# Performance work log

Hardware: AMD Instinct MI355X
Metric: run time of the kernel (lower is better)

## Reference

```python
import jax, jax.numpy as jnp
import numpy as np
import math

DIM = 1024
N_HEADS = 16
HEAD_DIM = DIM // N_HEADS  # 64
GROUP = 128
B, T = 2, 2048
ROPE_THETA = 10000.0


def bitlinear(x, w, group_size=GROUP):
    """BitLinear (BitNet b1.58 style) forward: per-group ternary weight quant +
    per-token int8 absmax activation quant. STE is irrelevant in fwd-only."""
    O, I = w.shape
    wg = w.reshape(O, I // group_size, group_size)
    ws = jnp.mean(jnp.abs(wg), axis=-1, keepdims=True) + 1e-5
    wq = (jnp.clip(jnp.round(wg / ws), -1.0, 1.0) * ws).reshape(O, I)
    s = 127.0 / (jnp.max(jnp.abs(x), axis=-1, keepdims=True) + 1e-5)
    xq = jnp.clip(jnp.round(x * s), -128.0, 127.0) / s
    return jnp.einsum('bti,oi->bto', xq, wq)


def rope(x, cos, sin):
    # x: [B,T,H,D]; cos/sin: [T,D/2]; complex mult on interleaved pairs
    xs = x.reshape(*x.shape[:-1], -1, 2)
    xe, xo = xs[..., 0], xs[..., 1]
    c = cos[None, :, None, :]
    s = sin[None, :, None, :]
    oe = xe * c - xo * s
    oo = xe * s + xo * c
    return jnp.stack([oe, oo], axis=-1).reshape(x.shape)


def setup_inputs() -> dict:
    key = jax.random.key(0)
    ks = jax.random.split(key, 5)
    x = jax.random.normal(ks[0], (B, T, DIM), dtype=jnp.float32)
    wq_w = jax.random.normal(ks[1], (DIM, DIM), dtype=jnp.float32) * 0.02
    wk_w = jax.random.normal(ks[2], (DIM, DIM), dtype=jnp.float32) * 0.02
    wv_w = jax.random.normal(ks[3], (DIM, DIM), dtype=jnp.float32) * 0.02
    wo_w = jax.random.normal(ks[4], (DIM, DIM), dtype=jnp.float32) * 0.02
    # precompute freqs_cis (as cos/sin) like standard RoPE
    inv = 1.0 / (ROPE_THETA ** (np.arange(0, HEAD_DIM, 2, dtype=np.float32) / HEAD_DIM))
    ang = np.arange(T, dtype=np.float32)[:, None] * inv[None, :]  # [T, D/2]
    return {
        'x': x,
        'cos': jnp.asarray(np.cos(ang)),
        'sin': jnp.asarray(np.sin(ang)),
        'wq_w': wq_w, 'wk_w': wk_w, 'wv_w': wv_w, 'wo_w': wo_w,
    }


def reference(x, cos, sin, wq_w, wk_w, wv_w, wo_w):
    Bb, Tt, _ = x.shape
    q = bitlinear(x, wq_w).reshape(Bb, Tt, N_HEADS, HEAD_DIM)
    k = bitlinear(x, wk_w).reshape(Bb, Tt, N_HEADS, HEAD_DIM)
    v = bitlinear(x, wv_w).reshape(Bb, Tt, N_HEADS, HEAD_DIM)
    q = rope(q, cos, sin)
    k = rope(k, cos, sin)
    # [B,H,T,D]
    q = q.transpose(0, 2, 1, 3)
    k = k.transpose(0, 2, 1, 3)
    v = v.transpose(0, 2, 1, 3)
    attn = jnp.einsum('bhqd,bhkd->bhqk', q, k) / math.sqrt(HEAD_DIM)
    causal = jnp.tril(jnp.ones((Tt, Tt), dtype=bool))
    attn = jnp.where(causal[None, None], attn, -jnp.inf)
    attn = jax.nn.softmax(attn, axis=-1)
    out = jnp.einsum('bhqk,bhkd->bhqd', attn, v)
    out = out.transpose(0, 2, 1, 3).reshape(Bb, Tt, -1)
    return bitlinear(out, wo_w)
```

## Files before the change

kernel.cpp:

```cpp
#include <hip/hip_runtime.h>
#include <math.h>

#define DIM   1024
#define NH    16
#define HD    64
#define GRP   128
#define BB    2
#define TT    2048
#define MROWS (BB*TT)

typedef __attribute__((ext_vector_type(8))) short s16x8;
typedef __attribute__((ext_vector_type(4))) float f32x4;
typedef __attribute__((ext_vector_type(4))) int   i32x4;
typedef __attribute__((ext_vector_type(16))) int  i32x16;

__device__ inline float wave_max(float v){
    for(int off=32; off; off>>=1) v = fmaxf(v, __shfl_xor(v, off));
    return v;
}

__device__ inline unsigned short f2bf(float x){
    union { float f; unsigned u; } v; v.f = x;
    unsigned r = v.u + 0x7fffu + ((v.u >> 16) & 1u);
    return (unsigned short)(r >> 16);
}

#if __has_builtin(__builtin_amdgcn_cvt_pk_bf16_f32)
typedef __bf16 bf16x2 __attribute__((ext_vector_type(2)));
__device__ inline unsigned pk2(float a, float b){
    union { bf16x2 v; unsigned u; } c;
    c.v = __builtin_amdgcn_cvt_pk_bf16_f32(a, b);
    return c.u;
}
#else
__device__ inline unsigned pk2(float a, float b){
    return (unsigned)f2bf(a) | ((unsigned)f2bf(b) << 16);
}
#endif

#if __has_builtin(__builtin_amdgcn_exp2f)
__device__ inline float fexp2(float x){ return __builtin_amdgcn_exp2f(x); }
#else
__device__ inline float fexp2(float x){ return exp2f(x); }
#endif

__device__ inline i32x16 zero16(){
    i32x16 z;
    #pragma unroll
    for(int i=0;i<16;i++) z[i]=0;
    return z;
}

__device__ inline void gload16(const void* g, void* l){
    __builtin_amdgcn_global_load_lds((const __attribute__((address_space(1))) unsigned int*)g,
                                     (__attribute__((address_space(3))) unsigned int*)l, 16, 0, 0);
}

__global__ __launch_bounds__(256) void quant_w4(const float* __restrict__ w0,
                                                const float* __restrict__ w1,
                                                const float* __restrict__ w2,
                                                const float* __restrict__ w3,
                                                char* __restrict__ w8,
                                                float* __restrict__ wsall){
    int blk = blockIdx.x;
    int widx = blk >> 8;
    const float* w = (widx==0)?w0 : (widx==1)?w1 : (widx==2)?w2 : w3;
    int tid = threadIdx.x;
    int gloc = (blk & 255)*32 + (tid >> 3);
    int j = tid & 7;
    const float* p = w + (size_t)gloc*GRP;
    float r = 0.f;
    #pragma unroll
    for(int i=0;i<16;i++) r += fabsf(p[8*i + j]);
    r += __shfl_xor(r, 1);
    r += __shfl_xor(r, 2);
    r += __shfl_xor(r, 4);
    float ws = r/(float)GRP + 1e-5f;
    if (j == 0) wsall[widx*8192 + gloc] = ws;
    int* q = (int*)(w8 + (size_t)widx*1048576 + (size_t)gloc*GRP);
    int i0 = j*16;
    #pragma unroll
    for(int c4=0;c4<4;c4++){
        float4 v = *(const float4*)(p + i0 + c4*4);
        int b0 = (int)fminf(fmaxf(rintf(v.x/ws),-1.f),1.f);
        int b1 = (int)fminf(fmaxf(rintf(v.y/ws),-1.f),1.f);
        int b2 = (int)fminf(fmaxf(rintf(v.z/ws),-1.f),1.f);
        int b3 = (int)fminf(fmaxf(rintf(v.w/ws),-1.f),1.f);
        q[j*4 + c4] = (b0&0xff) | ((b1&0xff)<<8) | ((b2&0xff)<<16) | ((b3&0xff)<<24);
    }
}

__global__ __launch_bounds__(256) void quant_x_i8(const float* __restrict__ x,
                                                  char* __restrict__ xq8,
                                                  float* __restrict__ srow){
    int row = blockIdx.x;
    int tid = threadIdx.x;
    const float* p = x + (size_t)row*DIM;
    float4 v = *(const float4*)(p + tid*4);
    float m = fmaxf(fmaxf(fabsf(v.x),fabsf(v.y)), fmaxf(fabsf(v.z),fabsf(v.w)));
    m = wave_max(m);
    __shared__ float red[4];
    if ((tid&63)==0) red[tid>>6] = m;
    __syncthreads();
    m = fmaxf(fmaxf(red[0],red[1]), fmaxf(red[2],red[3]));
    float s = 127.f/(m+1e-5f);
    int a0 = (int)fminf(fmaxf(rintf(v.x*s),-128.f),127.f);
    int a1 = (int)fminf(fmaxf(rintf(v.y*s),-128.f),127.f);
    int a2 = (int)fminf(fmaxf(rintf(v.z*s),-128.f),127.f);
    int a3 = (int)fminf(fmaxf(rintf(v.w*s),-128.f),127.f);
    int pk = (a0&0xff) | ((a1&0xff)<<8) | ((a2&0xff)<<16) | ((a3&0xff)<<24);
    ((int*)xq8)[(size_t)row*256 + tid] = pk;
    if (tid==0) srow[row] = s;
}

__global__ __launch_bounds__(256) void gemm_i8(const char* __restrict__ A8,
                                               const char* __restrict__ W8,
                                               const float* __restrict__ wsb,
                                               const float* __restrict__ srow,
                                               float* __restrict__ C){
    __shared__ __align__(16) char As[2][8192];
    __shared__ __align__(16) char Bs[2][16384];
    int tid = threadIdx.x;
    int w = tid >> 6, lane = tid & 63;
    int wm = w & 1, wn = w >> 1;
    int m0 = blockIdx.y*64, n0 = blockIdx.x*128;
    int l31 = lane & 31, lh = lane >> 5;

    float wsr[2][8];
    #pragma unroll
    for(int jt=0; jt<2; jt++){
        int col = n0 + (wn*2+jt)*32 + l31;
        float4 q0 = *(const float4*)(wsb + (size_t)col*8);
        float4 q1 = *(const float4*)(wsb + (size_t)col*8 + 4);
        wsr[jt][0]=q0.x; wsr[jt][1]=q0.y; wsr[jt][2]=q0.z; wsr[jt][3]=q0.w;
        wsr[jt][4]=q1.x; wsr[jt][5]=q1.y; wsr[jt][6]=q1.z; wsr[jt][7]=q1.w;
    }

    float facc[2][16];
    #pragma unroll
    for(int b=0;b<2;b++)
        #pragma unroll
        for(int r=0;r<16;r++) facc[b][r]=0.f;

    int row8 = lane >> 3;
    int scw  = (lane&7) ^ ((lane>>3)&7);
    const char* Ab = A8 + (size_t)m0*1024;
    const char* Bb = W8 + (size_t)n0*1024;

    {
        #pragma unroll
        for(int r=0;r<2;r++){
            int j = w*2 + r;
            gload16(Ab + (size_t)(j*8 + row8)*1024 + scw*16, As[0] + j*1024);
        }
        #pragma unroll
        for(int r=0;r<4;r++){
            int j = w*4 + r;
            gload16(Bb + (size_t)(j*8 + row8)*1024 + scw*16, Bs[0] + j*1024);
        }
    }

    #pragma unroll
    for(int g=0; g<8; g++){
        __syncthreads();
        if (g+1 < 8){
            int nb = (g+1)&1;
            #pragma unroll
            for(int r=0;r<2;r++){
                int j = w*2 + r;
                gload16(Ab + (size_t)(j*8 + row8)*1024 + (g+1)*128 + scw*16, As[nb] + j*1024);
            }
            #pragma unroll
            for(int r=0;r<4;r++){
                int j = w*4 + r;
                gload16(Bb + (size_t)(j*8 + row8)*1024 + (g+1)*128 + scw*16, Bs[nb] + j*1024);
            }
        }
        const char* Ac = As[g&1];
        const char* Bc = Bs[g&1];

        i32x16 iacc[2];
        iacc[0]=zero16(); iacc[1]=zero16();
        #pragma unroll
        for(int s=0; s<4; s++){
            int cw = s*2 + lh;
            int rlA = wm*32 + l31;
            i32x4 afr = *(const i32x4*)(Ac + (rlA*8 + (cw ^ (rlA&7)))*16);
            #pragma unroll
            for(int jt=0; jt<2; jt++){
                int rlB = (wn*2+jt)*32 + l31;
                i32x4 bfr = *(const i32x4*)(Bc + (rlB*8 + (cw ^ (rlB&7)))*16);
                iacc[jt] = __builtin_amdgcn_mfma_i32_32x32x32_i8(afr, bfr, iacc[jt], 0, 0, 0);
            }
        }
        #pragma unroll
        for(int jt=0; jt<2; jt++)
            #pragma unroll
            for(int r=0;r<16;r++)
                facc[jt][r] += (float)iacc[jt][r] * wsr[jt][g];
    }

    #pragma unroll
    for(int r=0; r<16; r++){
        int rowl = wm*32 + (r&3) + 8*(r>>2) + 4*lh;
        float sv = srow[m0 + rowl];
        #pragma unroll
        for(int jt=0; jt<2; jt++){
            int col = n0 + (wn*2+jt)*32 + l31;
            C[(size_t)(m0+rowl)*DIM + col] = facc[jt][r] / sv;
        }
    }
}

#define QSC 0.18033688011112042f
__global__ __launch_bounds__(256) void pack_qk(const float* __restrict__ qb,
                                               const float* __restrict__ kb,
                                               const float* __restrict__ cosb,
                                               const float* __restrict__ sinb,
                                               unsigned short* __restrict__ Qh,
                                               char* __restrict__ Kf){
    int idx = blockIdx.x*blockDim.x + threadIdx.x;
    int bt = idx >> 9;
    int r  = idx & 511;
    int h  = r >> 5;
    int p  = r & 31;
    int b  = bt >> 11;
    int t  = bt & (TT-1);
    int bh = b*NH + h;
    float c = cosb[t*32+p], s = sinb[t*32+p];
    size_t src = (size_t)bt*DIM + h*HD + 2*p;
    float q0 = qb[src], q1 = qb[src+1];
    float k0 = kb[src], k1 = kb[src+1];
    float qe = (q0*c - q1*s)*QSC, qo = (q0*s + q1*c)*QSC;
    float ke = k0*c - k1*s,       ko = k0*s + k1*c;
    size_t qdst = ((size_t)bh*TT + t)*HD + 2*p;
    *(ushort2*)(Qh + qdst) = make_ushort2(f2bf(qe), f2bf(qo));
    int kt = t >> 6, tl = t & 63;
    int f = tl >> 4, mm = tl & 15;
    int cc = p >> 4, gg = (p >> 2) & 3, j2 = (p & 3)*2;
    size_t kdst = ((size_t)(bh*32 + kt)*512 + f*128 + cc*64 + gg*16 + mm)*16 + j2*2;
    *(ushort2*)(Kf + kdst) = make_ushort2(f2bf(ke), f2bf(ko));
}

__global__ __launch_bounds__(256) void pack_v(const float* __restrict__ vb,
                                              char* __restrict__ Vf){
    __shared__ float st[64][65];
    int blk = blockIdx.x;
    int kt = blk & 31;
    int bh = blk >> 5;
    int b  = bh >> 4;
    int h  = bh & 15;
    int tid = threadIdx.x;
    #pragma unroll
    for(int rep=0; rep<16; rep++){
        int idx = rep*256 + tid;
        int tl = idx >> 6, dv = idx & 63;
        st[tl][dv] = vb[(size_t)(b*TT + kt*64 + tl)*DIM + h*HD + dv];
    }
    __syncthreads();
    char* base = Vf + ((size_t)blk*512)*16;
    #pragma unroll
    for(int rep=0; rep<2; rep++){
        int e = rep*256 + tid;
        int f = e >> 7, cc = (e >> 6) & 1, gg = (e >> 4) & 3, mm = e & 15;
        int dv = 16*f + mm;
        int tb = 8*gg + 32*cc;
        unsigned short sh[8];
        #pragma unroll
        for(int j=0;j<8;j++) sh[j] = f2bf(st[tb+j][dv]);
        *(s16x8*)(base + (size_t)e*16) = *(s16x8*)sh;
    }
}

__global__ __launch_bounds__(256) void attn_mfma3(const unsigned short* __restrict__ Qh,
                                                  const char* __restrict__ Kf,
                                                  const char* __restrict__ Vf,
                                                  float* __restrict__ ao){
    __shared__ s16x8 Kbuf[2][512];
    __shared__ s16x8 Vbuf[2][512];
    int blk = blockIdx.x;
    int qt = 31 - (blk >> 5);
    int bh = blk & 31;
    int b  = bh >> 4;
    int tid = threadIdx.x;
    int w = tid >> 6, lane = tid & 63;
    int m = lane & 15, g = lane >> 4;
    int q = qt*64 + w*16 + m;

    const unsigned short* Qhead = Qh + (size_t)bh*TT*HD;
    const char* Kbase = Kf + (size_t)bh*32*8192;
    const char* Vbase = Vf + (size_t)bh*32*8192;

    s16x8 Qf0 = *(const s16x8*)(Qhead + (size_t)q*HD + g*8);
    s16x8 Qf1 = *(const s16x8*)(Qhead + (size_t)q*HD + g*8 + 32);

    f32x4 Of[4] = {f32x4{0,0,0,0}, f32x4{0,0,0,0}, f32x4{0,0,0,0}, f32x4{0,0,0,0}};
    float mrow = -1e30f, lrow = 0.f;

    #pragma unroll
    for(int r=0;r<2;r++){
        gload16(Kbase + ((r*4 + w)*64 + lane)*16, (char*)Kbuf[0] + (r*4 + w)*1024);
        gload16(Vbase + ((r*4 + w)*64 + lane)*16, (char*)Vbuf[0] + (r*4 + w)*1024);
    }

    for(int kt=0; kt<=qt; kt++){
        __syncthreads();
        if (kt < qt){
            int nb = (kt+1)&1;
            size_t goff = (size_t)(kt+1)*8192;
            #pragma unroll
            for(int r=0;r<2;r++){
                gload16(Kbase + goff + ((r*4 + w)*64 + lane)*16, (char*)Kbuf[nb] + (r*4 + w)*1024);
                gload16(Vbase + goff + ((r*4 + w)*64 + lane)*16, (char*)Vbuf[nb] + (r*4 + w)*1024);
            }
        }
        const s16x8* Kc = Kbuf[kt&1];
        const s16x8* Vc = Vbuf[kt&1];

        f32x4 S[4];
        #pragma unroll
        for(int f=0; f<4; f++){
            s16x8 k0 = Kc[(f*2+0)*64 + lane];
            s16x8 k1 = Kc[(f*2+1)*64 + lane];
            f32x4 acc = {0,0,0,0};
            acc = __builtin_amdgcn_mfma_f32_16x16x32_bf16(k0, Qf0, acc, 0, 0, 0);
            acc = __builtin_amdgcn_mfma_f32_16x16x32_bf16(k1, Qf1, acc, 0, 0, 0);
            S[f] = acc;
        }

        float p[4][4];
        float mloc = -1e30f;
        if (kt == qt){
            #pragma unroll
            for(int f=0; f<4; f++)
                #pragma unroll
                for(int r=0; r<4; r++){
                    int key = 16*f + 4*g + r;
                    float s = (qt*64 + key > q) ? -1e30f : S[f][r];
                    p[f][r] = s;
                    mloc = fmaxf(mloc, s);
                }
        } else {
            #pragma unroll
            for(int f=0; f<4; f++)
                #pragma unroll
                for(int r=0; r<4; r++){
                    p[f][r] = S[f][r];
                    mloc = fmaxf(mloc, S[f][r]);
                }
        }
        mloc = fmaxf(mloc, __shfl_xor(mloc, 16));
        mloc = fmaxf(mloc, __shfl_xor(mloc, 32));
        float mn = fmaxf(mrow, mloc);
        float alpha = fexp2(mrow - mn);
        float ps = 0.f;
        #pragma unroll
        for(int f=0; f<4; f++)
            #pragma unroll
            for(int r=0; r<4; r++){
                float e = fexp2(p[f][r] - mn);
                p[f][r] = e;
                ps += e;
            }
        ps += __shfl_xor(ps, 16);
        ps += __shfl_xor(ps, 32);
        lrow = lrow*alpha + ps;
        mrow = mn;

        #pragma unroll
        for(int f2=0; f2<4; f2++)
            #pragma unroll
            for(int r=0; r<4; r++) Of[f2][r] *= alpha;

        unsigned pp0[4], pp1[4];
        #pragma unroll
        for(int f=0; f<4; f++){
            pp0[f] = pk2(p[f][0], p[f][1]);
            pp1[f] = pk2(p[f][2], p[f][3]);
        }

        int src0 = m + 16*(2*(g&1));
        int src1 = src0 + 16;
        bool hi = (g >= 2);
        #pragma unroll
        for(int c=0; c<2; c++){
            unsigned a0 = (unsigned)__shfl((int)pp0[2*c],   src0);
            unsigned a1 = (unsigned)__shfl((int)pp0[2*c+1], src0);
            unsigned b0 = hi ? a1 : a0;
            unsigned a2 = (unsigned)__shfl((int)pp1[2*c],   src0);
            unsigned a3 = (unsigned)__shfl((int)pp1[2*c+1], src0);
            unsigned b1 = hi ? a3 : a2;
            unsigned a4 = (unsigned)__shfl((int)pp0[2*c],   src1);
            unsigned a5 = (unsigned)__shfl((int)pp0[2*c+1], src1);
            unsigned b2 = hi ? a5 : a4;
            unsigned a6 = (unsigned)__shfl((int)pp1[2*c],   src1);
            unsigned a7 = (unsigned)__shfl((int)pp1[2*c+1], src1);
            unsigned b3 = hi ? a7 : a6;
            union { unsigned u[4]; s16x8 v; } Bf;
            Bf.u[0]=b0; Bf.u[1]=b1; Bf.u[2]=b2; Bf.u[3]=b3;
            #pragma unroll
            for(int f2=0; f2<4; f2++){
                s16x8 vf = Vc[(f2*2+c)*64 + lane];
                Of[f2] = __builtin_amdgcn_mfma_f32_16x16x32_bf16(vf, Bf.v, Of[f2], 0, 0, 0);
            }
        }
    }

    float invl = 1.0f / lrow;
    size_t obase = (size_t)(b*TT + q)*DIM + (bh & 15)*HD;
    #pragma unroll
    for(int f2=0; f2<4; f2++)
        #pragma unroll
        for(int r=0; r<4; r++)
            ao[obase + 16*f2 + 4*g + r] = Of[f2][r]*invl;
}

extern "C" void kernel_launch(void* const* d_in, const int* in_sizes, int n_in,
                              void* d_out, int out_size, void* d_ws, size_t ws_size,
                              hipStream_t stream){
    const float* x    = (const float*)d_in[0];
    const float* cosb = (const float*)d_in[1];
    const float* sinb = (const float*)d_in[2];
    const float* wq_w = (const float*)d_in[3];
    const float* wk_w = (const float*)d_in[4];
    const float* wv_w = (const float*)d_in[5];
    const float* wo_w = (const float*)d_in[6];
    float* out = (float*)d_out;

    char*  cw = (char*)d_ws;
    const size_t MB = 1048576;
    char*  w8all = cw;
    float* wsall = (float*)(cw + 4*MB);
    float* srow1 = wsall + 4*8192;
    float* srow2 = srow1 + 4096;
    char*  xq8   = cw + 5*MB;
    char*  xq8_2 = cw + 9*MB;
    float* qb    = (float*)(cw + 13*MB);
    float* kb    = (float*)(cw + 29*MB);
    float* vb    = (float*)(cw + 45*MB);
    unsigned short* Qh = (unsigned short*)(cw + 61*MB);
    char*  Kf    = cw + 69*MB;
    char*  Vf    = cw + 13*MB;
    float* ao    = kb;

    quant_w4<<<1024, 256, 0, stream>>>(wq_w, wk_w, wv_w, wo_w, w8all, wsall);
    quant_x_i8<<<MROWS, 256, 0, stream>>>(x, xq8, srow1);

    dim3 gg(DIM/128, MROWS/64);
    gemm_i8<<<gg, 256, 0, stream>>>(xq8, w8all + 0*MB, wsall + 0*8192, srow1, qb);
    gemm_i8<<<gg, 256, 0, stream>>>(xq8, w8all + 1*MB, wsall + 1*8192, srow1, kb);
    gemm_i8<<<gg, 256, 0, stream>>>(xq8, w8all + 2*MB, wsall + 2*8192, srow1, vb);

    pack_qk<<<(MROWS*512)/256, 256, 0, stream>>>(qb, kb, cosb, sinb, Qh, Kf);
    pack_v<<<BB*NH*(TT/64), 256, 0, stream>>>(vb, Vf);

    attn_mfma3<<<1024, 256, 0, stream>>>(Qh, Kf, Vf, ao);

    quant_x_i8<<<MROWS, 256, 0, stream>>>(ao, xq8_2, srow2);
    gemm_i8<<<gg, 256, 0, stream>>>(xq8_2, w8all + 3*MB, wsall + 3*8192, srow2, out);
}
```

Measured before the change: 248.0 us.

## Fuse quant kernels, QKV GEMMs with RoPE/pack, and split-K causal attention

Merges weight and activation quantization into one launch. Fuses the three QKV GEMMs into a single grid whose epilogue applies RoPE and writes bf16 Q/K/V directly in the attention layouts, removing the fp32 intermediates and the pack kernels. Splits long causal query tiles into two key-range halves with a separate merge kernel to balance work across blocks. In exchange it adds scattered 2-byte stores in the GEMM epilogue and partial-result traffic for the merge.

```diff
diff --git a/kernel.cpp b/kernel.cpp
--- a/kernel.cpp
+++ b/kernel.cpp
@@ -56,37 +56,62 @@
                                      (__attribute__((address_space(3))) unsigned int*)l, 16, 0, 0);
 }
 
-__global__ __launch_bounds__(256) void quant_w4(const float* __restrict__ w0,
-                                                const float* __restrict__ w1,
-                                                const float* __restrict__ w2,
-                                                const float* __restrict__ w3,
-                                                char* __restrict__ w8,
-                                                float* __restrict__ wsall){
+#define QSC 0.18033688011112042f
+
+__global__ __launch_bounds__(256) void quant_all(const float* __restrict__ x,
+                                                 const float* __restrict__ w0,
+                                                 const float* __restrict__ w1,
+                                                 const float* __restrict__ w2,
+                                                 const float* __restrict__ w3,
+                                                 char* __restrict__ w8,
+                                                 float* __restrict__ wsall,
+                                                 char* __restrict__ xq8,
+                                                 float* __restrict__ srow){
     int blk = blockIdx.x;
-    int widx = blk >> 8;
-    const float* w = (widx==0)?w0 : (widx==1)?w1 : (widx==2)?w2 : w3;
     int tid = threadIdx.x;
-    int gloc = (blk & 255)*32 + (tid >> 3);
-    int j = tid & 7;
-    const float* p = w + (size_t)gloc*GRP;
-    float r = 0.f;
-    #pragma unroll
-    for(int i=0;i<16;i++) r += fabsf(p[8*i + j]);
-    r += __shfl_xor(r, 1);
-    r += __shfl_xor(r, 2);
-    r += __shfl_xor(r, 4);
-    float ws = r/(float)GRP + 1e-5f;
-    if (j == 0) wsall[widx*8192 + gloc] = ws;
-    int* q = (int*)(w8 + (size_t)widx*1048576 + (size_t)gloc*GRP);
-    int i0 = j*16;
-    #pragma unroll
-    for(int c4=0;c4<4;c4++){
-        float4 v = *(const float4*)(p + i0 + c4*4);
-        int b0 = (int)fminf(fmaxf(rintf(v.x/ws),-1.f),1.f);
-        int b1 = (int)fminf(fmaxf(rintf(v.y/ws),-1.f),1.f);
-        int b2 = (int)fminf(fmaxf(rintf(v.z/ws),-1.f),1.f);
-        int b3 = (int)fminf(fmaxf(rintf(v.w/ws),-1.f),1.f);
-        q[j*4 + c4] = (b0&0xff) | ((b1&0xff)<<8) | ((b2&0xff)<<16) | ((b3&0xff)<<24);
+    if (blk < 1024){
+        int widx = blk >> 8;
+        const float* w = (widx==0)?w0 : (widx==1)?w1 : (widx==2)?w2 : w3;
+        int gloc = (blk & 255)*32 + (tid >> 3);
+        int j = tid & 7;
+        const float* p = w + (size_t)gloc*GRP;
+        float r = 0.f;
+        #pragma unroll
+        for(int i=0;i<16;i++) r += fabsf(p[8*i + j]);
+        r += __shfl_xor(r, 1);
+        r += __shfl_xor(r, 2);
+        r += __shfl_xor(r, 4);
+        float ws = r/(float)GRP + 1e-5f;
+        if (j == 0) wsall[widx*8192 + gloc] = ws;
+        int* q = (int*)(w8 + (size_t)widx*1048576 + (size_t)gloc*GRP);
+        int i0 = j*16;
+        #pragma unroll
+        for(int c4=0;c4<4;c4++){
+            float4 v = *(const float4*)(p + i0 + c4*4);
+            int b0 = (int)fminf(fmaxf(rintf(v.x/ws),-1.f),1.f);
+            int b1 = (int)fminf(fmaxf(rintf(v.y/ws),-1.f),1.f);
+            int b2 = (int)fminf(fmaxf(rintf(v.z/ws),-1.f),1.f);
+            int b3 = (int)fminf(fmaxf(rintf(v.w/ws),-1.f),1.f);
+            q[j*4 + c4] = (b0&0xff) | ((b1&0xff)<<8) | ((b2&0xff)<<16) | ((b3&0xff)<<24);
+        }
+    } else {
+        int row = blk - 1024;
+        const float* p = x + (size_t)row*DIM;
+        float4 v = *(const float4*)(p + tid*4);
+        float m = fmaxf(fmaxf(fabsf(v.x),fabsf(v.y)), fmaxf(fabsf(v.z),fabsf(v.w)));
+        m = wave_max(m);
+        __shared__ float red[4];
+        if ((tid&63)==0) red[tid>>6] = m;
+        __syncthreads();
+        m = fmaxf(fmaxf(red[0],red[1]), fmaxf(red[2],red[3]));
+        float s = 127.f/(m+1e-5f);
+        int a0 = (int)fminf(fmaxf(rintf(v.x*s),-128.f),127.f);
+        int a1 = (int)fminf(fmaxf(rintf(v.y*s),-128.f),127.f);
+        int a2 = (int)fminf(fmaxf(rintf(v.z*s),-128.f),127.f);
+        int a3 = (int)fminf(fmaxf(rintf(v.w*s),-128.f),127.f);
+        int pk = (a0&0xff) | ((a1&0xff)<<8) | ((a2&0xff)<<16) | ((a3&0xff)<<24);
+        ((int*)xq8)[(size_t)row*256 + tid] = pk;
+        if (tid==0) srow[row] = s;
     }
 }
 
@@ -113,6 +138,161 @@
     if (tid==0) srow[row] = s;
 }
 
+__global__ __launch_bounds__(256) void gemm_qkv(const char* __restrict__ A8,
+                                                const char* __restrict__ w8all,
+                                                const float* __restrict__ wsall,
+                                                const float* __restrict__ srow,
+                                                const float* __restrict__ cosb,
+                                                const float* __restrict__ sinb,
+                                                unsigned short* __restrict__ Qh,
+                                                unsigned short* __restrict__ Kf,
+                                                unsigned short* __restrict__ Vf){
+    __shared__ __align__(16) char As[2][8192];
+    __shared__ __align__(16) char Bs[2][16384];
+    int nt = blockIdx.x;
+    int widx = nt >> 3;
+    int n0 = (nt & 7)*128;
+    int m0 = blockIdx.y*64;
+    const char* W8 = w8all + (size_t)widx*1048576;
+    const float* wsb = wsall + widx*8192;
+
+    int tid = threadIdx.x;
+    int w = tid >> 6, lane = tid & 63;
+    int wm = w & 1, wn = w >> 1;
+    int l31 = lane & 31, lh = lane >> 5;
+
+    float wsr[2][8];
+    #pragma unroll
+    for(int jt=0; jt<2; jt++){
+        int col = n0 + (wn*2+jt)*32 + l31;
+        float4 q0 = *(const float4*)(wsb + (size_t)col*8);
+        float4 q1 = *(const float4*)(wsb + (size_t)col*8 + 4);
+        wsr[jt][0]=q0.x; wsr[jt][1]=q0.y; wsr[jt][2]=q0.z; wsr[jt][3]=q0.w;
+        wsr[jt][4]=q1.x; wsr[jt][5]=q1.y; wsr[jt][6]=q1.z; wsr[jt][7]=q1.w;
+    }
+
+    float facc[2][16];
+    #pragma unroll
+    for(int b=0;b<2;b++)
+        #pragma unroll
+        for(int r=0;r<16;r++) facc[b][r]=0.f;
+
+    int row8 = lane >> 3;
+    int scw  = (lane&7) ^ ((lane>>3)&7);
+    const char* Ab = A8 + (size_t)m0*1024;
+    const char* Bb = W8 + (size_t)n0*1024;
+
+    {
+        #pragma unroll
+        for(int r=0;r<2;r++){
+            int j = w*2 + r;
+            gload16(Ab + (size_t)(j*8 + row8)*1024 + scw*16, As[0] + j*1024);
+        }
+        #pragma unroll
+        for(int r=0;r<4;r++){
+            int j = w*4 + r;
+            gload16(Bb + (size_t)(j*8 + row8)*1024 + scw*16, Bs[0] + j*1024);
+        }
+    }
+
+    #pragma unroll
+    for(int g=0; g<8; g++){
+        __syncthreads();
+        if (g+1 < 8){
+            int nb = (g+1)&1;
+            #pragma unroll
+            for(int r=0;r<2;r++){
+                int j = w*2 + r;
+                gload16(Ab + (size_t)(j*8 + row8)*1024 + (g+1)*128 + scw*16, As[nb] + j*1024);
+            }
+            #pragma unroll
+            for(int r=0;r<4;r++){
+                int j = w*4 + r;
+                gload16(Bb + (size_t)(j*8 + row8)*1024 + (g+1)*128 + scw*16, Bs[nb] + j*1024);
+            }
+        }
+        const char* Ac = As[g&1];
+        const char* Bc = Bs[g&1];
+
+        i32x16 iacc[2];
+        iacc[0]=zero16(); iacc[1]=zero16();
+        #pragma unroll
+        for(int s=0; s<4; s++){
+            int cw = s*2 + lh;
+            int rlA = wm*32 + l31;
+            i32x4 afr = *(const i32x4*)(Ac + (rlA*8 + (cw ^ (rlA&7)))*16);
+            #pragma unroll
+            for(int jt=0; jt<2; jt++){
+                int rlB = (wn*2+jt)*32 + l31;
+                i32x4 bfr = *(const i32x4*)(Bc + (rlB*8 + (cw ^ (rlB&7)))*16);
+                iacc[jt] = __builtin_amdgcn_mfma_i32_32x32x32_i8(afr, bfr, iacc[jt], 0, 0, 0);
+            }
+        }
+        #pragma unroll
+        for(int jt=0; jt<2; jt++)
+            #pragma unroll
+            for(int r=0;r<16;r++)
+                facc[jt][r] += (float)iacc[jt][r] * wsr[jt][g];
+    }
+
+    float fin[2][16];
+    #pragma unroll
+    for(int r=0; r<16; r++){
+        int rowl = wm*32 + (r&3) + 8*(r>>2) + 4*lh;
+        float sv = srow[m0 + rowl];
+        #pragma unroll
+        for(int jt=0; jt<2; jt++) fin[jt][r] = facc[jt][r] / sv;
+    }
+
+    int kt = (m0 & (TT-1)) >> 6;
+    int bglob = m0 >> 11;
+
+    if (widx == 2){
+        #pragma unroll
+        for(int jt=0; jt<2; jt++){
+            int col = n0 + (wn*2+jt)*32 + l31;
+            int h = col >> 6, d = col & 63;
+            int bh = bglob*NH + h;
+            size_t tb = ((size_t)(bh*32 + kt))*512;
+            int e = (d>>4)*128 + wm*64 + (d&15);
+            #pragma unroll
+            for(int rb=0; rb<4; rb++){
+                unsigned short s4[4];
+                #pragma unroll
+                for(int i=0;i<4;i++) s4[i] = f2bf(fin[jt][rb*4+i]);
+                *(ushort2*)(Vf + (tb + e + rb*16)*8 + 4*lh)     = *(ushort2*)&s4[0];
+                *(ushort2*)(Vf + (tb + e + rb*16)*8 + 4*lh + 2) = *(ushort2*)&s4[2];
+            }
+        }
+    } else {
+        #pragma unroll
+        for(int jt=0; jt<2; jt++){
+            int col = n0 + (wn*2+jt)*32 + l31;
+            int h = col >> 6, d = col & 63, p = d >> 1;
+            int bh = bglob*NH + h;
+            bool odd = (d & 1);
+            #pragma unroll
+            for(int r=0; r<16; r++){
+                int rowl = wm*32 + (r&3) + 8*(r>>2) + 4*lh;
+                int t = (m0 + rowl) & (TT-1);
+                float c = cosb[t*32+p], s = sinb[t*32+p];
+                float own = fin[jt][r];
+                float part = __shfl_xor(own, 1);
+                float e = odd ? part : own;
+                float o = odd ? own  : part;
+                float val = odd ? (e*s + o*c) : (e*c - o*s);
+                if (widx == 0){
+                    Qh[((size_t)bh*TT + t)*HD + d] = f2bf(val*QSC);
+                } else {
+                    int f = rowl >> 4, mm = rowl & 15;
+                    size_t entry = ((size_t)(bh*32 + kt))*512 + f*128 + (p>>4)*64 + ((p>>2)&3)*16 + mm;
+                    Kf[entry*8 + (p&3)*2 + (d&1)] = f2bf(val);
+                }
+            }
+        }
+    }
+}
+
 __global__ __launch_bounds__(256) void gemm_i8(const char* __restrict__ A8,
                                                const char* __restrict__ W8,
                                                const float* __restrict__ wsb,
@@ -212,75 +392,24 @@
     }
 }
 
-#define QSC 0.18033688011112042f
-__global__ __launch_bounds__(256) void pack_qk(const float* __restrict__ qb,
-                                               const float* __restrict__ kb,
-                                               const float* __restrict__ cosb,
-                                               const float* __restrict__ sinb,
-                                               unsigned short* __restrict__ Qh,
-                                               char* __restrict__ Kf){
-    int idx = blockIdx.x*blockDim.x + threadIdx.x;
-    int bt = idx >> 9;
-    int r  = idx & 511;
-    int h  = r >> 5;
-    int p  = r & 31;
-    int b  = bt >> 11;
-    int t  = bt & (TT-1);
-    int bh = b*NH + h;
-    float c = cosb[t*32+p], s = sinb[t*32+p];
-    size_t src = (size_t)bt*DIM + h*HD + 2*p;
-    float q0 = qb[src], q1 = qb[src+1];
-    float k0 = kb[src], k1 = kb[src+1];
-    float qe = (q0*c - q1*s)*QSC, qo = (q0*s + q1*c)*QSC;
-    float ke = k0*c - k1*s,       ko = k0*s + k1*c;
-    size_t qdst = ((size_t)bh*TT + t)*HD + 2*p;
-    *(ushort2*)(Qh + qdst) = make_ushort2(f2bf(qe), f2bf(qo));
-    int kt = t >> 6, tl = t & 63;
-    int f = tl >> 4, mm = tl & 15;
-    int cc = p >> 4, gg = (p >> 2) & 3, j2 = (p & 3)*2;
-    size_t kdst = ((size_t)(bh*32 + kt)*512 + f*128 + cc*64 + gg*16 + mm)*16 + j2*2;
-    *(ushort2*)(Kf + kdst) = make_ushort2(f2bf(ke), f2bf(ko));
-}
-
-__global__ __launch_bounds__(256) void pack_v(const float* __restrict__ vb,
-                                              char* __restrict__ Vf){
-    __shared__ float st[64][65];
-    int blk = blockIdx.x;
-    int kt = blk & 31;
-    int bh = blk >> 5;
-    int b  = bh >> 4;
-    int h  = bh & 15;
-    int tid = threadIdx.x;
-    #pragma unroll
-    for(int rep=0; rep<16; rep++){
-        int idx = rep*256 + tid;
-        int tl = idx >> 6, dv = idx & 63;
-        st[tl][dv] = vb[(size_t)(b*TT + kt*64 + tl)*DIM + h*HD + dv];
-    }
-    __syncthreads();
-    char* base = Vf + ((size_t)blk*512)*16;
-    #pragma unroll
-    for(int rep=0; rep<2; rep++){
-        int e = rep*256 + tid;
-        int f = e >> 7, cc = (e >> 6) & 1, gg = (e >> 4) & 3, mm = e & 15;
-        int dv = 16*f + mm;
-        int tb = 8*gg + 32*cc;
-        unsigned short sh[8];
-        #pragma unroll
-        for(int j=0;j<8;j++) sh[j] = f2bf(st[tb+j][dv]);
-        *(s16x8*)(base + (size_t)e*16) = *(s16x8*)sh;
-    }
-}
-
-__global__ __launch_bounds__(256) void attn_mfma3(const unsigned short* __restrict__ Qh,
-                                                  const char* __restrict__ Kf,
-                                                  const char* __restrict__ Vf,
-                                                  float* __restrict__ ao){
+__global__ __launch_bounds__(256) void attn_mfma4(const unsigned short* __restrict__ Qh,
+                                                  const unsigned short* __restrict__ Kf,
+                                                  const unsigned short* __restrict__ Vf,
+                                                  float* __restrict__ ao,
+                                                  float* __restrict__ Po,
+                                                  float* __restrict__ Pm,
+                                                  float* __restrict__ Pl){
     __shared__ s16x8 Kbuf[2][512];
     __shared__ s16x8 Vbuf[2][512];
     int blk = blockIdx.x;
-    int qt = 31 - (blk >> 5);
     int bh = blk & 31;
+    int s_ = blk >> 5;
+    int part = (s_ >= 32);
+    int qt = part ? (63 - s_) : (31 - s_);
+    int h1 = (qt < 16) ? (qt + 1) : ((qt + 1) >> 1);
+    int k0 = part ? h1 : 0;
+    int k1 = part ? (qt + 1) : h1;
+    int n = k1 - k0;
     int b  = bh >> 4;
     int tid = threadIdx.x;
     int w = tid >> 6, lane = tid & 63;
@@ -288,8 +417,8 @@
     int q = qt*64 + w*16 + m;
 
     const unsigned short* Qhead = Qh + (size_t)bh*TT*HD;
-    const char* Kbase = Kf + (size_t)bh*32*8192;
-    const char* Vbase = Vf + (size_t)bh*32*8192;
+    const s16x8* Kbase = (const s16x8*)(Kf + (size_t)bh*32*4096);
+    const s16x8* Vbase = (const s16x8*)(Vf + (size_t)bh*32*4096);
 
     s16x8 Qf0 = *(const s16x8*)(Qhead + (size_t)q*HD + g*8);
     s16x8 Qf1 = *(const s16x8*)(Qhead + (size_t)q*HD + g*8 + 32);
@@ -299,32 +428,34 @@
 
     #pragma unroll
     for(int r=0;r<2;r++){
-        gload16(Kbase + ((r*4 + w)*64 + lane)*16, (char*)Kbuf[0] + (r*4 + w)*1024);
-        gload16(Vbase + ((r*4 + w)*64 + lane)*16, (char*)Vbuf[0] + (r*4 + w)*1024);
-    }
-
-    for(int kt=0; kt<=qt; kt++){
+        gload16((const char*)(Kbase + (size_t)k0*512) + ((r*4 + w)*64 + lane)*16, (char*)Kbuf[0] + (r*4 + w)*1024);
+        gload16((const char*)(Vbase + (size_t)k0*512) + ((r*4 + w)*64 + lane)*16, (char*)Vbuf[0] + (r*4 + w)*1024);
+    }
+
+    for(int i=0; i<n; i++){
+        int kt = k0 + i;
         __syncthreads();
-        if (kt < qt){
-            int nb = (kt+1)&1;
-            size_t goff = (size_t)(kt+1)*8192;
+        if (i+1 < n){
+            int nb = (i+1)&1;
+            const char* kg = (const char*)(Kbase + (size_t)(kt+1)*512);
+            const char* vg = (const char*)(Vbase + (size_t)(kt+1)*512);
             #pragma unroll
             for(int r=0;r<2;r++){
-                gload16(Kbase + goff + ((r*4 + w)*64 + lane)*16, (char*)Kbuf[nb] + (r*4 + w)*1024);
-                gload16(Vbase + goff + ((r*4 + w)*64 + lane)*16, (char*)Vbuf[nb] + (r*4 + w)*1024);
-            }
-        }
-        const s16x8* Kc = Kbuf[kt&1];
-        const s16x8* Vc = Vbuf[kt&1];
+                gload16(kg + ((r*4 + w)*64 + lane)*16, (char*)Kbuf[nb] + (r*4 + w)*1024);
+                gload16(vg + ((r*4 + w)*64 + lane)*16, (char*)Vbuf[nb] + (r*4 + w)*1024);
+            }
+        }
+        const s16x8* Kc = Kbuf[i&1];
+        const s16x8* Vc = Vbuf[i&1];
 
         f32x4 S[4];
         #pragma unroll
         for(int f=0; f<4; f++){
-            s16x8 k0 = Kc[(f*2+0)*64 + lane];
-            s16x8 k1 = Kc[(f*2+1)*64 + lane];
+            s16x8 kk0 = Kc[(f*2+0)*64 + lane];
+            s16x8 kk1 = Kc[(f*2+1)*64 + lane];
             f32x4 acc = {0,0,0,0};
-            acc = __builtin_amdgcn_mfma_f32_16x16x32_bf16(k0, Qf0, acc, 0, 0, 0);
-            acc = __builtin_amdgcn_mfma_f32_16x16x32_bf16(k1, Qf1, acc, 0, 0, 0);
+            acc = __builtin_amdgcn_mfma_f32_16x16x32_bf16(kk0, Qf0, acc, 0, 0, 0);
+            acc = __builtin_amdgcn_mfma_f32_16x16x32_bf16(kk1, Qf1, acc, 0, 0, 0);
             S[f] = acc;
         }
 
@@ -336,9 +467,9 @@
                 #pragma unroll
                 for(int r=0; r<4; r++){
                     int key = 16*f + 4*g + r;
-                    float s = (qt*64 + key > q) ? -1e30f : S[f][r];
-                    p[f][r] = s;
-                    mloc = fmaxf(mloc, s);
+                    float sv = (qt*64 + key > q) ? -1e30f : S[f][r];
+                    p[f][r] = sv;
+                    mloc = fmaxf(mloc, sv);
                 }
         } else {
             #pragma unroll
@@ -406,13 +537,62 @@
         }
     }
 
-    float invl = 1.0f / lrow;
-    size_t obase = (size_t)(b*TT + q)*DIM + (bh & 15)*HD;
-    #pragma unroll
-    for(int f2=0; f2<4; f2++)
-        #pragma unroll
-        for(int r=0; r<4; r++)
-            ao[obase + 16*f2 + 4*g + r] = Of[f2][r]*invl;
+    if (qt < 16){
+        float invl = 1.0f / lrow;
+        size_t obase = (size_t)(b*TT + q)*DIM + (bh & 15)*HD;
+        #pragma unroll
+        for(int f2=0; f2<4; f2++)
+            #pragma unroll
+            for(int r=0; r<4; r++)
+                ao[obase + 16*f2 + 4*g + r] = Of[f2][r]*invl;
+    } else {
+        int si = (bh*16 + (qt-16))*2 + part;
+        float* Ob = Po + (size_t)si*4096 + (w*16 + m)*64;
+        #pragma unroll
+        for(int f2=0; f2<4; f2++)
+            #pragma unroll
+            for(int r=0; r<4; r++)
+                Ob[16*f2 + 4*g + r] = Of[f2][r];
+        if (g == 0){
+            Pm[si*64 + w*16 + m] = mrow;
+            Pl[si*64 + w*16 + m] = lrow;
+        }
+    }
+}
+
+__global__ __launch_bounds__(256) void attn_merge(const float* __restrict__ Po,
+                                                  const float* __restrict__ Pm,
+                                                  const float* __restrict__ Pl,
+                                                  float* __restrict__ ao){
+    int blk = blockIdx.x;
+    int bh = blk >> 4;
+    int qti = blk & 15;
+    int qt = 16 + qti;
+    int b = bh >> 4, h = bh & 15;
+    int tid = threadIdx.x;
+    int row = tid >> 2;
+    int d0 = (tid & 3)*16;
+    int si = (bh*16 + qti)*2;
+    float m1 = Pm[si*64 + row],     l1 = Pl[si*64 + row];
+    float m2 = Pm[(si+1)*64 + row], l2 = Pl[(si+1)*64 + row];
+    float mm = fmaxf(m1, m2);
+    float w1 = fexp2(m1 - mm), w2 = fexp2(m2 - mm);
+    float inv = 1.0f / (w1*l1 + w2*l2);
+    const float* O1 = Po + (size_t)si*4096 + row*64 + d0;
+    const float* O2 = Po + (size_t)(si+1)*4096 + row*64 + d0;
+    int q = qt*64 + row;
+    float* outp = ao + (size_t)(b*TT + q)*DIM + h*HD + d0;
+    #pragma unroll
+    for(int c=0; c<4; c++){
+        float4 v1 = *(const float4*)(O1 + c*4);
+        float4 v2 = *(const float4*)(O2 + c*4);
+        float4 o;
+        o.x = (v1.x*w1 + v2.x*w2)*inv;
+        o.y = (v1.y*w1 + v2.y*w2)*inv;
+        o.z = (v1.z*w1 + v2.z*w2)*inv;
+        o.w = (v1.w*w1 + v2.w*w2)*inv;
+        *(float4*)(outp + c*4) = o;
+    }
 }
 
 extern "C" void kernel_launch(void* const* d_in, const int* in_sizes, int n_in,
@@ -427,35 +607,32 @@
     const float* wo_w = (const float*)d_in[6];
     float* out = (float*)d_out;
 
-    char*  cw = (char*)d_ws;
+    char* cw = (char*)d_ws;
     const size_t MB = 1048576;
     char*  w8all = cw;
     float* wsall = (float*)(cw + 4*MB);
-    float* srow1 = wsall + 4*8192;
-    float* srow2 = srow1 + 4096;
+    float* srow1 = (float*)(cw + 4*MB + 131072);
+    float* srow2 = (float*)(cw + 4*MB + 147456);
     char*  xq8   = cw + 5*MB;
     char*  xq8_2 = cw + 9*MB;
-    float* qb    = (float*)(cw + 13*MB);
-    float* kb    = (float*)(cw + 29*MB);
-    float* vb    = (float*)(cw + 45*MB);
-    unsigned short* Qh = (unsigned short*)(cw + 61*MB);
-    char*  Kf    = cw + 69*MB;
-    char*  Vf    = cw + 13*MB;
-    float* ao    = kb;
-
-    quant_w4<<<1024, 256, 0, stream>>>(wq_w, wk_w, wv_w, wo_w, w8all, wsall);
-    quant_x_i8<<<MROWS, 256, 0, stream>>>(x, xq8, srow1);
-
-    dim3 gg(DIM/128, MROWS/64);
-    gemm_i8<<<gg, 256, 0, stream>>>(xq8, w8all + 0*MB, wsall + 0*8192, srow1, qb);
-    gemm_i8<<<gg, 256, 0, stream>>>(xq8, w8all + 1*MB, wsall + 1*8192, srow1, kb);
-    gemm_i8<<<gg, 256, 0, stream>>>(xq8, w8all + 2*MB, wsall + 2*8192, srow1, vb);
-
-    pack_qk<<<(MROWS*512)/256, 256, 0, stream>>>(qb, kb, cosb, sinb, Qh, Kf);
-    pack_v<<<BB*NH*(TT/64), 256, 0, stream>>>(vb, Vf);
-
-    attn_mfma3<<<1024, 256, 0, stream>>>(Qh, Kf, Vf, ao);
+    unsigned short* Qh = (unsigned short*)(cw + 13*MB);
+    unsigned short* Kf = (unsigned short*)(cw + 21*MB);
+    unsigned short* Vf = (unsigned short*)(cw + 29*MB);
+    float* ao    = (float*)(cw + 37*MB);
+    float* Po    = (float*)(cw + 53*MB);
+    float* Pm    = (float*)(cw + 70*MB);
+    float* Pl    = (float*)(cw + 70*MB + 262144);
+
+    quant_all<<<1024 + MROWS, 256, 0, stream>>>(x, wq_w, wk_w, wv_w, wo_w,
+                                                w8all, wsall, xq8, srow1);
+
+    gemm_qkv<<<dim3(24, MROWS/64), 256, 0, stream>>>(xq8, w8all, wsall, srow1,
+                                                     cosb, sinb, Qh, Kf, Vf);
+
+    attn_mfma4<<<1536, 256, 0, stream>>>(Qh, Kf, Vf, ao, Po, Pm, Pl);
+    attn_merge<<<512, 256, 0, stream>>>(Po, Pm, Pl, ao);
 
     quant_x_i8<<<MROWS, 256, 0, stream>>>(ao, xq8_2, srow2);
-    gemm_i8<<<gg, 256, 0, stream>>>(xq8_2, w8all + 3*MB, wsall + 3*8192, srow2, out);
-}
+    gemm_i8<<<dim3(DIM/128, MROWS/64), 256, 0, stream>>>(xq8_2, w8all + 3*MB,
+                                                         wsall + 3*8192, srow2, out);
+}
```

Result: slower. 262.0 us (+5.6%).
